# Kernel optimization log

Measured on AMD Instinct MI355X. Metric: run time of the kernel, lower is better.

Reference implementation:

```python
import jax, jax.numpy as jnp
import numpy as np

E, S, D_IN, D_LAT, D_HID = 1024, 64, 128, 128, 512
NSTEPS, DT = 8192, 0.01
KL_WEIGHT = 0.01


def setup_inputs() -> dict:
    key = jax.random.key(0)
    ks = jax.random.split(key, 12)
    sd = lambda fan_in: 1.0 / np.sqrt(fan_in)
    return {
        'event_marks': jax.random.normal(ks[0], (E, D_IN), jnp.float32),
        'z_events': jax.random.normal(ks[1], (E, S, D_LAT), jnp.float32),
        'z_traj': jax.random.normal(ks[2], (NSTEPS, S, D_LAT), jnp.float32),
        'times': jnp.arange(NSTEPS + 1, dtype=jnp.float32) * DT,
        'Wp': jax.random.normal(ks[3], (D_IN, D_LAT), jnp.float32) * sd(D_IN),
        'bp': jnp.zeros((D_LAT,), jnp.float32),
        'W1': jax.random.normal(ks[4], (D_LAT, D_HID), jnp.float32) * sd(D_LAT),
        'b1': jnp.zeros((D_HID,), jnp.float32),
        'W2': jax.random.normal(ks[5], (D_HID, 1), jnp.float32) * sd(D_HID),
        'b2': jnp.zeros((1,), jnp.float32),
        'base_intensity': jnp.asarray(0.1, jnp.float32),
        'Wd1': jax.random.normal(ks[6], (D_LAT, D_HID), jnp.float32) * sd(D_LAT),
        'bd1': jnp.zeros((D_HID,), jnp.float32),
        'Wd2': jax.random.normal(ks[7], (D_HID, D_LAT), jnp.float32) * sd(D_HID),
        'bd2': jnp.zeros((D_LAT,), jnp.float32),
    }


def reference(event_marks, z_events, z_traj, times, Wp, bp, W1, b1, W2, b2,
              base_intensity, Wd1, bd1, Wd2, bd2):
    # input projection of marks: [E, D_LAT]
    marks_proj = event_marks @ Wp + bp

    def intensity(z):  # z: [..., D_LAT] -> [...]
        h = jax.nn.relu(z @ W1 + b1)
        s = (h @ W2 + b2)[..., 0]
        return jax.nn.softplus(s + base_intensity)

    # log-intensity at events: sum over events of mean over samples
    lam_ev = intensity(z_events)                      # [E, S]
    log_intensity_sum = jnp.log(lam_ev + 1e-8).mean(axis=1).sum()

    # compensator integral over the trajectory (left Riemann sum)
    lam_traj = intensity(z_traj)                      # [NSTEPS, S]
    dts = jnp.diff(times)                             # [NSTEPS]
    integral = (lam_traj.mean(axis=1) * dts).sum()

    # Gaussian decoder log-prob: mu = MLP(z), unit variance
    h = jax.nn.relu(z_events @ Wd1 + bd1)             # [E, S, D_HID]
    mu = h @ Wd2 + bd2                                # [E, S, D_LAT]
    x = marks_proj[:, None, :]                        # [E, 1, D_LAT]
    log_2pi = jnp.log(jnp.asarray(2.0 * np.pi, jnp.float32))
    log_p = -0.5 * jnp.sum((x - mu) ** 2, axis=-1) - 0.5 * D_LAT * log_2pi  # [E, S]
    recon_loss = log_p.mean(axis=1).sum()

    kl_loss = KL_WEIGHT * jnp.mean(z_traj ** 2)

    elbo = log_intensity_sum - integral + recon_loss - kl_loss
    return -elbo
```

## Files before the change

### kernel.cpp

```cpp
#include <hip/hip_runtime.h>

typedef __attribute__((ext_vector_type(4))) float f32x4;
typedef __attribute__((ext_vector_type(8))) __bf16 bf16x8;
typedef __attribute__((ext_vector_type(4))) __bf16 bf16x4;

#define LOG_2PI 1.8378770664093453f

__device__ __forceinline__ float softplus_f(float x) {
  return fmaxf(x, 0.f) + log1pf(expf(-fabsf(x)));
}

__device__ __forceinline__ void barrier_lds_only() {
  asm volatile("s_waitcnt lgkmcnt(0)\n\ts_barrier" ::: "memory");
}

__global__ void prep_kernel(const float* __restrict__ em,
                            const float* __restrict__ Wp,
                            const float* __restrict__ bp,
                            float* __restrict__ mp,
                            float* __restrict__ accs) {
  const int b = blockIdx.x;
  if (b == 1024) {
    if (threadIdx.x < 8) accs[threadIdx.x] = 0.f;
    return;
  }
  const int d = threadIdx.x;
  float s = bp[d];
  const float* emr = em + b * 128;
#pragma unroll 4
  for (int k = 0; k < 128; ++k) s += emr[k] * Wp[k * 128 + d];
  mp[b * 128 + d] = s;
}

__global__ __launch_bounds__(512, 1) void intensity7_kernel(
    const float* __restrict__ z_traj, const float* __restrict__ z_ev,
    const float* __restrict__ W1, const float* __restrict__ b1,
    const float* __restrict__ W2, const float* __restrict__ b2,
    const float* __restrict__ base_i, const float* __restrict__ times,
    float* __restrict__ accs) {
  __shared__ __align__(16) __bf16 w1t[512 * 128];
  __shared__ __align__(16) float b1L[512];
  __shared__ __align__(16) float w2L[512];
  __shared__ float red[8][4];

  const int tid = threadIdx.x;
  const int wid = tid >> 6, lid = tid & 63;
  const int g = lid >> 4, q = lid & 15;

  const int gw = blockIdx.x * 8 + wid;
  const int t0 = gw * 9;

  f32x4 rz[2][4][2];
#define LOADT(TILE)                                                            \
  do {                                                                         \
    const float* zp = ((TILE) < 16384)                                         \
                          ? z_traj + (size_t)(TILE) * 4096                     \
                          : z_ev + (size_t)((TILE) - 16384) * 4096;            \
    _Pragma("unroll") for (int s = 0; s < 2; ++s) {                            \
      _Pragma("unroll") for (int kf = 0; kf < 4; ++kf) {                       \
        const float* pp = zp + (s * 16 + q) * 128 + kf * 32 + g * 8;           \
        rz[s][kf][0] = *(const f32x4*)pp;                                      \
        rz[s][kf][1] = *(const f32x4*)(pp + 4);                                \
      }                                                                        \
    }                                                                          \
  } while (0)
  LOADT(t0);

  {
    const float* wcol = W1 + tid;
    char* wb = (char*)w1t;
    const int colbase = tid * 256;
    const int sw = (tid & 7) << 4;
#pragma unroll 8
    for (int k = 0; k < 128; k += 2) {
      float a = wcol[(size_t)k * 512];
      float c = wcol[(size_t)(k + 1) * 512];
      union { __bf16 h[2]; unsigned u; } pk;
      pk.h[0] = (__bf16)a;
      pk.h[1] = (__bf16)c;
      *(unsigned*)(wb + (colbase + ((k * 2) ^ sw))) = pk.u;
    }
    b1L[tid] = b1[tid];
    w2L[tid] = W2[tid];
  }
  const float sbias = b2[0] + base_i[0];
  barrier_lds_only();

  float integral_loc = 0.f, logsum_loc = 0.f, kls = 0.f;
  const char* wb = (const char*)w1t;
  const int wsw = (q & 7) << 4;

#pragma unroll 1
  for (int i = 0; i < 9; ++i) {
    const int tile = t0 + i;
    const bool traj_t = (tile < 16384);

    bf16x8 fr[2][4];
#pragma unroll
    for (int s = 0; s < 2; ++s) {
#pragma unroll
      for (int kf = 0; kf < 4; ++kf) {
        f32x4 a0 = rz[s][kf][0], a1 = rz[s][kf][1];
        if (traj_t) {
          kls += a0[0] * a0[0] + a0[1] * a0[1] + a0[2] * a0[2] + a0[3] * a0[3];
          kls += a1[0] * a1[0] + a1[1] * a1[1] + a1[2] * a1[2] + a1[3] * a1[3];
        }
        bf16x8 f;
#pragma unroll
        for (int j = 0; j < 4; ++j) {
          f[j] = (__bf16)a0[j];
          f[4 + j] = (__bf16)a1[j];
        }
        fr[s][kf] = f;
      }
    }
    if (i < 8) LOADT(tile + 1);
    __builtin_amdgcn_sched_barrier(0);

    float rowacc0 = 0.f, rowacc1 = 0.f;
#pragma unroll 4
    for (int c = 0; c < 32; ++c) {
      f32x4 a0 = {}, a1 = {};
#pragma unroll
      for (int kf = 0; kf < 4; ++kf) {
        bf16x8 wf = *(const bf16x8*)(wb + c * 4096 + q * 256 +
                                     ((kf * 64 + g * 16) ^ wsw));
        a0 = __builtin_amdgcn_mfma_f32_16x16x32_bf16(wf, fr[0][kf], a0, 0, 0, 0);
        a1 = __builtin_amdgcn_mfma_f32_16x16x32_bf16(wf, fr[1][kf], a1, 0, 0, 0);
      }
      f32x4 bb = *(const f32x4*)&b1L[c * 16 + g * 4];
      f32x4 ww = *(const f32x4*)&w2L[c * 16 + g * 4];
#pragma unroll
      for (int ii = 0; ii < 4; ++ii) {
        rowacc0 += fmaxf(a0[ii] + bb[ii], 0.f) * ww[ii];
        rowacc1 += fmaxf(a1[ii] + bb[ii], 0.f) * ww[ii];
      }
    }
    rowacc0 += __shfl_xor(rowacc0, 16);
    rowacc0 += __shfl_xor(rowacc0, 32);
    rowacc1 += __shfl_xor(rowacc1, 16);
    rowacc1 += __shfl_xor(rowacc1, 32);

    if (lid < 32) {
      const float rs = (lid < 16) ? rowacc0 : rowacc1;
      const float lam = softplus_f(rs + sbias);
      if (traj_t) {
        const int R = tile * 32 + lid;
        const int ts = R >> 6;
        integral_loc += lam * (times[ts + 1] - times[ts]) * (1.f / 64.f);
      } else {
        logsum_loc += logf(lam + 1e-8f) * (1.f / 64.f);
      }
    }
  }
#undef LOADT

#pragma unroll
  for (int m = 32; m >= 1; m >>= 1) {
    integral_loc += __shfl_xor(integral_loc, m);
    logsum_loc += __shfl_xor(logsum_loc, m);
    kls += __shfl_xor(kls, m);
  }
  if (lid == 0) {
    red[wid][0] = integral_loc;
    red[wid][1] = logsum_loc;
    red[wid][2] = kls;
  }
  __syncthreads();
  if (tid == 0) {
    float I = 0.f, L = 0.f, K = 0.f;
#pragma unroll
    for (int w = 0; w < 8; ++w) {
      I += red[w][0];
      L += red[w][1];
      K += red[w][2];
    }
    atomicAdd(&accs[0], I);
    atomicAdd(&accs[1], L);
    atomicAdd(&accs[3], K);
  }
}

__global__ __launch_bounds__(512, 2) void decoder2_kernel(
    const float* __restrict__ z,
    const float* __restrict__ Wd1, const float* __restrict__ bd1,
    const float* __restrict__ Wd2, const float* __restrict__ bd2,
    const float* __restrict__ mp, float* __restrict__ recon_acc) {
  __shared__ __align__(16) __bf16 zbuf[2][32 * 128];
  __shared__ __align__(16) __bf16 hbuf[32 * 512];
  __shared__ float s_part[32][9];
  __shared__ float red[8];

  const int tid = threadIdx.x;
  const int wid = tid >> 6, lid = tid & 63;
  const int g = lid >> 4, q = lid & 15;
  const int cb = wid * 64;
  const int tile0 = blockIdx.x * 8;

  bf16x8 bw1[4][4];
  f32x4 bd1v[4];
#pragma unroll
  for (int cf = 0; cf < 4; ++cf) {
    const int col = cb + cf * 16 + q;
#pragma unroll
    for (int i = 0; i < 4; ++i) bd1v[cf][i] = bd1[cb + cf * 16 + g * 4 + i];
#pragma unroll
    for (int kf = 0; kf < 4; ++kf) {
      bf16x8 f;
#pragma unroll
      for (int j = 0; j < 8; ++j) f[j] = (__bf16)Wd1[(kf * 32 + g * 8 + j) * 512 + col];
      bw1[cf][kf] = f;
    }
  }
  const int dimf = wid * 16 + q;
  bf16x8 bw2[16];
#pragma unroll
  for (int kf2 = 0; kf2 < 16; ++kf2) {
    bf16x8 f;
#pragma unroll
    for (int j = 0; j < 8; ++j) f[j] = (__bf16)Wd2[(kf2 * 32 + g * 8 + j) * 128 + dimf];
    bw2[kf2] = f;
  }
  f32x4 bd2v;
#pragma unroll
  for (int i = 0; i < 4; ++i) bd2v[i] = bd2[wid * 16 + g * 4 + i];

  const int srow = tid >> 4, sk8 = (tid & 15) * 8;
  const int stg_byte = ((srow * 256 + sk8 * 2) ^ ((srow & 7) << 4));
  char* hb = (char*)hbuf;

  float local = 0.f;

  {
    const float* p = z + (size_t)tile0 * 4096 + tid * 8;
    f32x4 r0 = *(const f32x4*)p, r1 = *(const f32x4*)(p + 4);
    bf16x8 v;
#pragma unroll
    for (int j = 0; j < 4; ++j) { v[j] = (__bf16)r0[j]; v[4 + j] = (__bf16)r1[j]; }
    *(bf16x8*)((char*)zbuf[0] + stg_byte) = v;
  }
  f32x4 rA0, rA1, rB0, rB1;
  { const float* p = z + (size_t)(tile0 + 1) * 4096 + tid * 8; rA0 = *(const f32x4*)p; rA1 = *(const f32x4*)(p + 4); }
  { const float* p = z + (size_t)(tile0 + 2) * 4096 + tid * 8; rB0 = *(const f32x4*)p; rB1 = *(const f32x4*)(p + 4); }
  barrier_lds_only();

#define DBODY(T, ZC, RR0, RR1)                                                     \
  do {                                                                             \
    f32x4 acc1[2][4] = {};                                                         \
    char* zc = (char*)zbuf[ZC];                                                    \
    _Pragma("unroll") for (int kf = 0; kf < 4; ++kf) {                             \
      _Pragma("unroll") for (int rf = 0; rf < 2; ++rf) {                           \
        const int row = rf * 16 + q;                                               \
        bf16x8 a = *(const bf16x8*)(zc + ((row * 256 + kf * 64 + g * 16) ^ ((row & 7) << 4))); \
        _Pragma("unroll") for (int cf = 0; cf < 4; ++cf)                           \
          acc1[rf][cf] = __builtin_amdgcn_mfma_f32_16x16x32_bf16(bw1[cf][kf], a, acc1[rf][cf], 0, 0, 0); \
      }                                                                            \
    }                                                                              \
    {                                                                              \
      bf16x8 v;                                                                    \
      _Pragma("unroll") for (int j = 0; j < 4; ++j) { v[j] = (__bf16)RR0[j]; v[4 + j] = (__bf16)RR1[j]; } \
      *(bf16x8*)((char*)zbuf[(ZC) ^ 1] + stg_byte) = v;                            \
    }                                                                              \
    {                                                                              \
      int tl = (T) + 3; if (tl > 7) tl = 7;                                        \
      const float* p = z + (size_t)(tile0 + tl) * 4096 + tid * 8;                  \
      RR0 = *(const f32x4*)p; RR1 = *(const f32x4*)(p + 4);                        \
    }                                                                              \
    _Pragma("unroll") for (int rf = 0; rf < 2; ++rf) {                             \
      const int row = rf * 16 + q;                                                 \
      _Pragma("unroll") for (int cf = 0; cf < 4; ++cf) {                           \
        bf16x4 hv;                                                                 \
        _Pragma("unroll") for (int i = 0; i < 4; ++i)                              \
          hv[i] = (__bf16)fmaxf(acc1[rf][cf][i] + bd1v[cf][i], 0.f);               \
        const int byt = ((row * 1024 + (cb + cf * 16 + g * 4) * 2) ^ ((row & 7) << 4)); \
        *(bf16x4*)(hb + byt) = hv;                                                 \
      }                                                                            \
    }                                                                              \
    barrier_lds_only();                                                            \
    f32x4 acc2[2] = {};                                                            \
    _Pragma("unroll") for (int kf2 = 0; kf2 < 16; ++kf2) {                         \
      _Pragma("unroll") for (int rf2 = 0; rf2 < 2; ++rf2) {                        \
        const int row = rf2 * 16 + q;                                              \
        bf16x8 a = *(const bf16x8*)(hb + ((row * 1024 + kf2 * 64 + g * 16) ^ ((row & 7) << 4))); \
        acc2[rf2] = __builtin_amdgcn_mfma_f32_16x16x32_bf16(bw2[kf2], a, acc2[rf2], 0, 0, 0); \
      }                                                                            \
    }                                                                              \
    const int e = (tile0 + (T)) >> 1;                                              \
    _Pragma("unroll") for (int rf2 = 0; rf2 < 2; ++rf2) {                          \
      float partial = 0.f;                                                         \
      _Pragma("unroll") for (int i = 0; i < 4; ++i) {                              \
        const float xv = mp[e * 128 + wid * 16 + g * 4 + i];                       \
        const float d = xv - (acc2[rf2][i] + bd2v[i]);                             \
        partial += d * d;                                                          \
      }                                                                            \
      partial += __shfl_xor(partial, 16);                                          \
      partial += __shfl_xor(partial, 32);                                          \
      if (lid < 16) s_part[rf2 * 16 + lid][wid] = partial;                         \
    }                                                                              \
    barrier_lds_only();                                                            \
    if (tid < 32) {                                                                \
      float t2 = 0.f;                                                              \
      _Pragma("unroll") for (int w = 0; w < 8; ++w) t2 += s_part[tid][w];          \
      local += (-0.5f * t2 - 0.5f * 128.f * LOG_2PI) * (1.f / 64.f);               \
    }                                                                              \
  } while (0)

#pragma unroll 1
  for (int t = 0; t < 8; t += 2) {
    DBODY(t, 0, rA0, rA1);
    DBODY(t + 1, 1, rB0, rB1);
  }
#undef DBODY

  if (wid == 0) {
#pragma unroll
    for (int m = 16; m >= 1; m >>= 1) local += __shfl_xor(local, m);
    if (lid == 0) atomicAdd(recon_acc, local);
  }
}

__global__ void finalize_kernel(const float* __restrict__ accs, float* __restrict__ out) {
  const float kl = 0.01f * (accs[3] / 67108864.f);
  const float elbo = accs[1] - accs[0] + accs[2] - kl;
  out[0] = -elbo;
}

extern "C" void kernel_launch(void* const* d_in, const int* in_sizes, int n_in,
                              void* d_out, int out_size, void* d_ws, size_t ws_size,
                              hipStream_t stream) {
  const float* event_marks = (const float*)d_in[0];
  const float* z_events = (const float*)d_in[1];
  const float* z_traj = (const float*)d_in[2];
  const float* times = (const float*)d_in[3];
  const float* Wp = (const float*)d_in[4];
  const float* bp = (const float*)d_in[5];
  const float* W1 = (const float*)d_in[6];
  const float* b1 = (const float*)d_in[7];
  const float* W2 = (const float*)d_in[8];
  const float* b2 = (const float*)d_in[9];
  const float* base_i = (const float*)d_in[10];
  const float* Wd1 = (const float*)d_in[11];
  const float* bd1 = (const float*)d_in[12];
  const float* Wd2 = (const float*)d_in[13];
  const float* bd2 = (const float*)d_in[14];

  float* mp = (float*)d_ws;
  float* accs = (float*)((char*)d_ws + 1024 * 128 * 4);

  prep_kernel<<<1025, 128, 0, stream>>>(event_marks, Wp, bp, mp, accs);
  intensity7_kernel<<<256, 512, 0, stream>>>(z_traj, z_events, W1, b1, W2, b2,
                                             base_i, times, accs);
  decoder2_kernel<<<256, 512, 0, stream>>>(z_events, Wd1, bd1, Wd2, bd2, mp,
                                           &accs[2]);
  finalize_kernel<<<1, 1, 0, stream>>>(accs, (float*)d_out);
}
```

Measured before the change: 151.6 us.

## Widen intensity blocks to 12 waves, 64-row tiles, and split decoder grid

The intensity kernel now runs 768 threads (12 waves) per block. Each wave processes 64-row tiles, one full timestep with four MFMA accumulator chains, using a grid-stride loop instead of a fixed 9-tile register-prefetch schedule. The explicit next-tile register prefetch is removed, so latency hiding now relies on more resident waves and more independent MFMA chains. The decoder grid doubles to 512 blocks of 4 tiles each, to spread work across more CUs.

```diff
diff --git a/kernel.cpp b/kernel.cpp
--- a/kernel.cpp
+++ b/kernel.cpp
@@ -32,7 +32,7 @@
   mp[b * 128 + d] = s;
 }
 
-__global__ __launch_bounds__(512, 1) void intensity7_kernel(
+__global__ __launch_bounds__(768, 3) void intensity8_kernel(
     const float* __restrict__ z_traj, const float* __restrict__ z_ev,
     const float* __restrict__ W1, const float* __restrict__ b1,
     const float* __restrict__ W2, const float* __restrict__ b2,
@@ -41,32 +41,13 @@
   __shared__ __align__(16) __bf16 w1t[512 * 128];
   __shared__ __align__(16) float b1L[512];
   __shared__ __align__(16) float w2L[512];
-  __shared__ float red[8][4];
+  __shared__ float red[12][4];
 
   const int tid = threadIdx.x;
   const int wid = tid >> 6, lid = tid & 63;
   const int g = lid >> 4, q = lid & 15;
 
-  const int gw = blockIdx.x * 8 + wid;
-  const int t0 = gw * 9;
-
-  f32x4 rz[2][4][2];
-#define LOADT(TILE)                                                            \
-  do {                                                                         \
-    const float* zp = ((TILE) < 16384)                                         \
-                          ? z_traj + (size_t)(TILE) * 4096                     \
-                          : z_ev + (size_t)((TILE) - 16384) * 4096;            \
-    _Pragma("unroll") for (int s = 0; s < 2; ++s) {                            \
-      _Pragma("unroll") for (int kf = 0; kf < 4; ++kf) {                       \
-        const float* pp = zp + (s * 16 + q) * 128 + kf * 32 + g * 8;           \
-        rz[s][kf][0] = *(const f32x4*)pp;                                      \
-        rz[s][kf][1] = *(const f32x4*)(pp + 4);                                \
-      }                                                                        \
-    }                                                                          \
-  } while (0)
-  LOADT(t0);
-
-  {
+  if (tid < 512) {
     const float* wcol = W1 + tid;
     char* wb = (char*)w1t;
     const int colbase = tid * 256;
@@ -86,22 +67,31 @@
   const float sbias = b2[0] + base_i[0];
   barrier_lds_only();
 
+  const int gw = blockIdx.x * 12 + wid;
   float integral_loc = 0.f, logsum_loc = 0.f, kls = 0.f;
   const char* wb = (const char*)w1t;
   const int wsw = (q & 7) << 4;
 
 #pragma unroll 1
-  for (int i = 0; i < 9; ++i) {
-    const int tile = t0 + i;
-    const bool traj_t = (tile < 16384);
-
-    bf16x8 fr[2][4];
-#pragma unroll
-    for (int s = 0; s < 2; ++s) {
+  for (int p = gw; p < 9216; p += 3072) {
+    const bool traj_p = (p < 8192);
+    const float* zbase = traj_p ? (z_traj + (size_t)p * 8192)
+                                : (z_ev + (size_t)(p - 8192) * 8192);
+
+    bf16x8 fr[4][4];
+#pragma unroll
+    for (int s = 0; s < 4; ++s) {
+      const float* rp = zbase + (s * 16 + q) * 128 + g * 8;
+      f32x4 ld[4][2];
 #pragma unroll
       for (int kf = 0; kf < 4; ++kf) {
-        f32x4 a0 = rz[s][kf][0], a1 = rz[s][kf][1];
-        if (traj_t) {
+        ld[kf][0] = *(const f32x4*)(rp + kf * 32);
+        ld[kf][1] = *(const f32x4*)(rp + kf * 32 + 4);
+      }
+#pragma unroll
+      for (int kf = 0; kf < 4; ++kf) {
+        f32x4 a0 = ld[kf][0], a1 = ld[kf][1];
+        if (traj_p) {
           kls += a0[0] * a0[0] + a0[1] * a0[1] + a0[2] * a0[2] + a0[3] * a0[3];
           kls += a1[0] * a1[0] + a1[1] * a1[1] + a1[2] * a1[2] + a1[3] * a1[3];
         }
@@ -114,19 +104,19 @@
         fr[s][kf] = f;
       }
     }
-    if (i < 8) LOADT(tile + 1);
-    __builtin_amdgcn_sched_barrier(0);
-
-    float rowacc0 = 0.f, rowacc1 = 0.f;
-#pragma unroll 4
+
+    float rowacc0 = 0.f, rowacc1 = 0.f, rowacc2 = 0.f, rowacc3 = 0.f;
+#pragma unroll 2
     for (int c = 0; c < 32; ++c) {
-      f32x4 a0 = {}, a1 = {};
+      f32x4 a0 = {}, a1 = {}, a2 = {}, a3 = {};
 #pragma unroll
       for (int kf = 0; kf < 4; ++kf) {
         bf16x8 wf = *(const bf16x8*)(wb + c * 4096 + q * 256 +
                                      ((kf * 64 + g * 16) ^ wsw));
         a0 = __builtin_amdgcn_mfma_f32_16x16x32_bf16(wf, fr[0][kf], a0, 0, 0, 0);
         a1 = __builtin_amdgcn_mfma_f32_16x16x32_bf16(wf, fr[1][kf], a1, 0, 0, 0);
+        a2 = __builtin_amdgcn_mfma_f32_16x16x32_bf16(wf, fr[2][kf], a2, 0, 0, 0);
+        a3 = __builtin_amdgcn_mfma_f32_16x16x32_bf16(wf, fr[3][kf], a3, 0, 0, 0);
       }
       f32x4 bb = *(const f32x4*)&b1L[c * 16 + g * 4];
       f32x4 ww = *(const f32x4*)&w2L[c * 16 + g * 4];
@@ -134,26 +124,31 @@
       for (int ii = 0; ii < 4; ++ii) {
         rowacc0 += fmaxf(a0[ii] + bb[ii], 0.f) * ww[ii];
         rowacc1 += fmaxf(a1[ii] + bb[ii], 0.f) * ww[ii];
+        rowacc2 += fmaxf(a2[ii] + bb[ii], 0.f) * ww[ii];
+        rowacc3 += fmaxf(a3[ii] + bb[ii], 0.f) * ww[ii];
       }
     }
     rowacc0 += __shfl_xor(rowacc0, 16);
     rowacc0 += __shfl_xor(rowacc0, 32);
     rowacc1 += __shfl_xor(rowacc1, 16);
     rowacc1 += __shfl_xor(rowacc1, 32);
-
-    if (lid < 32) {
-      const float rs = (lid < 16) ? rowacc0 : rowacc1;
+    rowacc2 += __shfl_xor(rowacc2, 16);
+    rowacc2 += __shfl_xor(rowacc2, 32);
+    rowacc3 += __shfl_xor(rowacc3, 16);
+    rowacc3 += __shfl_xor(rowacc3, 32);
+
+    {
+      const int s = lid >> 4;
+      const float rs = (s == 0) ? rowacc0 : (s == 1) ? rowacc1
+                     : (s == 2) ? rowacc2 : rowacc3;
       const float lam = softplus_f(rs + sbias);
-      if (traj_t) {
-        const int R = tile * 32 + lid;
-        const int ts = R >> 6;
-        integral_loc += lam * (times[ts + 1] - times[ts]) * (1.f / 64.f);
+      if (traj_p) {
+        integral_loc += lam * (times[p + 1] - times[p]) * (1.f / 64.f);
       } else {
         logsum_loc += logf(lam + 1e-8f) * (1.f / 64.f);
       }
     }
   }
-#undef LOADT
 
 #pragma unroll
   for (int m = 32; m >= 1; m >>= 1) {
@@ -170,7 +165,7 @@
   if (tid == 0) {
     float I = 0.f, L = 0.f, K = 0.f;
 #pragma unroll
-    for (int w = 0; w < 8; ++w) {
+    for (int w = 0; w < 12; ++w) {
       I += red[w][0];
       L += red[w][1];
       K += red[w][2];
@@ -195,7 +190,7 @@
   const int wid = tid >> 6, lid = tid & 63;
   const int g = lid >> 4, q = lid & 15;
   const int cb = wid * 64;
-  const int tile0 = blockIdx.x * 8;
+  const int tile0 = blockIdx.x * 4;
 
   bf16x8 bw1[4][4];
   f32x4 bd1v[4];
@@ -262,7 +257,7 @@
       *(bf16x8*)((char*)zbuf[(ZC) ^ 1] + stg_byte) = v;                            \
     }                                                                              \
     {                                                                              \
-      int tl = (T) + 3; if (tl > 7) tl = 7;                                        \
+      int tl = (T) + 3; if (tl > 3) tl = 3;                                        \
       const float* p = z + (size_t)(tile0 + tl) * 4096 + tid * 8;                  \
       RR0 = *(const f32x4*)p; RR1 = *(const f32x4*)(p + 4);                        \
     }                                                                              \
@@ -306,7 +301,7 @@
   } while (0)
 
 #pragma unroll 1
-  for (int t = 0; t < 8; t += 2) {
+  for (int t = 0; t < 4; t += 2) {
     DBODY(t, 0, rA0, rA1);
     DBODY(t + 1, 1, rB0, rB1);
   }
@@ -348,9 +343,9 @@
   float* accs = (float*)((char*)d_ws + 1024 * 128 * 4);
 
   prep_kernel<<<1025, 128, 0, stream>>>(event_marks, Wp, bp, mp, accs);
-  intensity7_kernel<<<256, 512, 0, stream>>>(z_traj, z_events, W1, b1, W2, b2,
+  intensity8_kernel<<<256, 768, 0, stream>>>(z_traj, z_events, W1, b1, W2, b2,
                                              base_i, times, accs);
-  decoder2_kernel<<<256, 512, 0, stream>>>(z_events, Wd1, bd1, Wd2, bd2, mp,
+  decoder2_kernel<<<512, 512, 0, stream>>>(z_events, Wd1, bd1, Wd2, bd2, mp,
                                            &accs[2]);
   finalize_kernel<<<1, 1, 0, stream>>>(accs, (float*)d_out);
 }
```

Measured after the change: 148.3 us. 2.2% less time.
